# Kernel optimization log

Hardware: AMD Instinct MI355X
Metric: run time of the kernel (lower is better)

## Reference

```python
import jax, jax.numpy as jnp
import numpy as np

B, N, IN, E, OUT = 4, 128, 256, 128, 128
EPS = 1e-5
NEG = -1.0e9


def _ln(x, s, o):
    m = x.mean(-1, keepdims=True)
    v = ((x - m) ** 2).mean(-1, keepdims=True)
    return s * jax.lax.rsqrt(v + EPS) * (x - m) + o


def setup_inputs() -> dict:
    key = jax.random.key(0)
    ks = jax.random.split(key, 30)

    def w(k, i, o):
        return (jax.random.normal(k, (i, o), jnp.float32) / np.sqrt(i)).astype(jnp.float32)

    z_dense = jax.random.normal(ks[0], (B, N, IN), jnp.float32)
    e_dense = jax.random.normal(ks[1], (B, N, N, E), jnp.float32)
    graph_fts = jax.random.normal(ks[2], (B, IN // 2), jnp.float32)
    lengths = jax.random.randint(ks[3], (B,), N // 2, N + 1)
    mask = jnp.arange(N)[None, :] < lengths[:, None]  # (B,N) bool
    adj = jax.random.uniform(ks[4], (B, N, N)) < 0.3
    adj = (adj | jnp.eye(N, dtype=bool)[None]) & mask[:, :, None] & mask[:, None, :]
    return dict(
        z_dense=z_dense, e_dense=e_dense, graph_fts=graph_fts, mask=mask, adj_mat=adj,
        Wt1=w(ks[5], IN, 8), Wt2=w(ks[6], IN, 8), Wt3=w(ks[7], IN, 8),
        We1=w(ks[8], E, 8), We2=w(ks[9], E, 8), We3=w(ks[10], E, 8),
        Wg=w(ks[11], IN // 2, 8),
        Wm1=w(ks[12], IN, OUT), Wm2=w(ks[13], IN, OUT), Wme=w(ks[14], E, OUT), Wmg=w(ks[15], E, OUT),
        ln1_s=jnp.ones((OUT,), jnp.float32), ln1_o=jnp.zeros((OUT,), jnp.float32),
        Wmlp1=w(ks[16], OUT, OUT),
        ln2_s=jnp.ones((OUT,), jnp.float32), ln2_o=jnp.zeros((OUT,), jnp.float32),
        Wmlp2=w(ks[17], OUT, OUT),
        WU1=w(ks[18], IN, OUT), WU2=w(ks[19], OUT, OUT), WU3=w(ks[20], 8, OUT),
        lnf_s=jnp.ones((OUT,), jnp.float32), lnf_o=jnp.zeros((OUT,), jnp.float32),
    )


def reference(z_dense, e_dense, graph_fts, mask, adj_mat,
              Wt1, Wt2, Wt3, We1, We2, We3, Wg,
              Wm1, Wm2, Wme, Wmg,
              ln1_s, ln1_o, Wmlp1, ln2_s, ln2_o, Wmlp2,
              WU1, WU2, WU3, lnf_s, lnf_o):
    mN = mask[..., None]  # (B,N,1)
    # --- triplet messages ---
    tri_1 = jnp.where(mN, z_dense @ Wt1, 0.0)  # (B,N,8)
    tri_2 = jnp.where(mN, z_dense @ Wt2, 0.0)
    tri_3 = jnp.where(mN, z_dense @ Wt3, 0.0)
    tri_e1 = e_dense @ We1  # (B,N,N,8)
    tri_e2 = e_dense @ We2
    tri_e3 = e_dense @ We3
    tri_g = graph_fts @ Wg  # (B,8)
    # (B,N,N,N,8) 7-way broadcast sum (axes: b, i, j, k)
    tri = (tri_1[:, :, None, None, :] + tri_2[:, None, :, None, :] + tri_3[:, None, None, :, :]
           + tri_e1[:, :, :, None, :] + tri_e2[:, :, None, :, :] + tri_e3[:, None, :, :, :]
           + tri_g[:, None, None, None, :])
    msk_tri = mask[:, None, None, :] | mask[:, None, :, None] | mask[:, :, None, None]
    tri = jnp.where(msk_tri[..., None], tri, NEG)
    tri_pooled = tri.max(axis=1)  # (B,N,N,8) -- max over first node axis
    tri_msgs = jax.nn.relu(tri_pooled @ WU3)  # (B,N,N,OUT)

    # --- pairwise messages ---
    msg_1 = jnp.where(mN, z_dense @ Wm1, 0.0)  # (B,N,OUT)
    msg_2 = jnp.where(mN, z_dense @ Wm2, 0.0)
    msg_e = jnp.where(adj_mat[..., None], e_dense @ Wme, 0.0)  # (B,N,N,OUT)
    msg_g = graph_fts @ Wmg  # (B,OUT)
    msgs = msg_1[:, None, :, :] + msg_2[:, :, None, :] + msg_e + msg_g[:, None, None, :]
    # M[-1]: [LN, ReLU, Linear] x2
    x = jax.nn.relu(_ln(msgs, ln1_s, ln1_o)) @ Wmlp1
    x = jax.nn.relu(_ln(x, ln2_s, ln2_o)) @ Wmlp2
    msgs = jnp.where(adj_mat[..., None], x, NEG).max(axis=1)  # (B,N,OUT)

    ret = _ln(z_dense @ WU1 + msgs @ WU2, lnf_s, lnf_o)  # (B,N,OUT)
    return ret, msgs, tri_msgs
```

## Files before the change

### kernel.cpp

```cpp
#include <hip/hip_runtime.h>

#define BN   4
#define NN   128
#define INF  256
#define EF   128
#define OUTF 128
#define EPSF 1e-5f
#define NEGF -998244352.0f

typedef __attribute__((ext_vector_type(8))) short short8;
typedef __attribute__((ext_vector_type(4))) float f32x4;

#define MFMA16(a, b, c) __builtin_amdgcn_mfma_f32_16x16x32_bf16(a, b, c, 0, 0, 0)

__device__ __forceinline__ unsigned short f2bf(float f) {
    unsigned u = __float_as_uint(f);
    u += 0x7fffu + ((u >> 16) & 1u);
    return (unsigned short)(u >> 16);
}
__device__ __forceinline__ unsigned pack2(float a, float b) {
    return (unsigned)f2bf(a) | ((unsigned)f2bf(b) << 16);
}

constexpr size_t TRI1 = 0;
constexpr size_t TRI2 = 4096;
constexpr size_t TRI3 = 8192;
constexpr size_t MSG1 = 12288;
constexpr size_t MSG2 = 77824;
constexpr size_t ZWU1 = 143360;
constexpr size_t TRIG = 208896;
constexpr size_t MSGG = 209920;
constexpr size_t E1T  = 210944;
constexpr size_t E2T  = 735232;
constexpr size_t E3N  = 1259520;
constexpr size_t PREPF = 1783808;

constexpr int W1T_OFF  = 0;
constexpr int W2T_OFF  = 16384;
constexpr int WMET_OFF = 32768;

constexpr size_t O_RET = 0;
constexpr size_t O_MSG = 65536;
constexpr size_t O_TRI = 131072;

__device__ __forceinline__ int detect_int(const void* mask) {
    const unsigned char* m = (const unsigned char*)mask;
    return (m[1] | m[2] | m[3]) == 0 ? 1 : 0;
}
__device__ __forceinline__ bool rdbool(const void* p, size_t idx, int isInt) {
    if (isInt) return ((const int*)p)[idx] != 0;
    return ((const unsigned char*)p)[idx] != 0;
}

__global__ __launch_bounds__(256, 4) void k_pre(
    const float* __restrict__ z, const float* __restrict__ e, const void* __restrict__ mask,
    const float* __restrict__ Wt1, const float* __restrict__ Wt2, const float* __restrict__ Wt3,
    const float* __restrict__ Wm1, const float* __restrict__ Wm2, const float* __restrict__ WU1,
    const float* __restrict__ g, const float* __restrict__ Wg, const float* __restrict__ Wmg,
    const float* __restrict__ W1, const float* __restrict__ W2, const float* __restrict__ Wme,
    const float* __restrict__ We1, const float* __restrict__ We2, const float* __restrict__ We3,
    float* __restrict__ ws, unsigned short* __restrict__ prep)
{
    int bx = blockIdx.x, tid = threadIdx.x;
    __shared__ __align__(16) unsigned char smem[128 * 136 * 2];

    if (bx < 512) {
        unsigned short* Ab = (unsigned short*)smem;
        int bi = bx;
        int b = bi >> 7, i = bi & 127;
        int lane = tid & 63, w = tid >> 6, q = lane >> 4, n = lane & 15;
        {
            int half = lane >> 5, c4 = (lane & 31) * 4;
            #pragma unroll
            for (int it = 0; it < 16; it++) {
                int row = 32 * w + 2 * it + half;
                float4 v = *(const float4*)(e + (size_t)bi * 16384 + (size_t)row * 128 + c4);
                unsigned* dst = (unsigned*)&Ab[row * 136 + c4];
                dst[0] = pack2(v.x, v.y);
                dst[1] = pack2(v.z, v.w);
            }
        }
        short8 bfrag[4][2];
        {
            #pragma unroll
            for (int t = 0; t < 2; t++) {
                int col = 16 * t + n;
                const float* Wsel = (col < 8) ? We1 : (col < 16 ? We2 : We3);
                int csel = col & 7;
                float mval = (col < 24) ? 1.f : 0.f;
                #pragma unroll
                for (int ks = 0; ks < 4; ks++) {
                    union { short8 s; unsigned short u[8]; } tmp;
                    #pragma unroll
                    for (int jj = 0; jj < 8; jj++) {
                        int k = ks * 32 + q * 8 + jj;
                        tmp.u[jj] = f2bf(Wsel[k * 8 + csel] * mval);
                    }
                    bfrag[ks][t] = tmp.s;
                }
            }
        }
        __builtin_amdgcn_wave_barrier();

        f32x4 ac2[2][2];
        #pragma unroll
        for (int rt = 0; rt < 2; rt++)
            #pragma unroll
            for (int t = 0; t < 2; t++) ac2[rt][t] = 0.f;
        #pragma unroll
        for (int ks = 0; ks < 4; ks++) {
            int k0 = ks * 32 + q * 8;
            short8 a0 = *(const short8*)&Ab[(32 * w + n) * 136 + k0];
            short8 a1 = *(const short8*)&Ab[(32 * w + 16 + n) * 136 + k0];
            #pragma unroll
            for (int t = 0; t < 2; t++) {
                ac2[0][t] = MFMA16(a0, bfrag[ks][t], ac2[0][t]);
                ac2[1][t] = MFMA16(a1, bfrag[ks][t], ac2[1][t]);
            }
        }
        #pragma unroll
        for (int rt = 0; rt < 2; rt++)
            #pragma unroll
            for (int reg = 0; reg < 4; reg++) {
                int row = 32 * w + 16 * rt + 4 * q + reg;
                float v0 = ac2[rt][0][reg];
                if (n < 8) ws[E1T + ((size_t)(b * 128 + row) * 128 + i) * 8 + n] = v0;
                else       ws[E2T + ((size_t)(b * 128 + row) * 128 + i) * 8 + (n - 8)] = v0;
                if (n < 8) ws[E3N + ((size_t)bi * 128 + row) * 8 + n] = ac2[rt][1][reg];
            }
        return;
    }
    if (bx < 1024) {
        int bn = bx - 512;
        int isInt = detect_int(mask);
        float* zr = (float*)smem;
        zr[tid] = z[(size_t)bn * INF + tid];
        __syncthreads();
        float mk = rdbool(mask, bn, isInt) ? 1.f : 0.f;
        for (int idx = tid; idx < 408; idx += 256) {
            const float* W; int c; size_t dst; int width; bool msk;
            if (idx < 8)        { W = Wt1; c = idx;       dst = TRI1 + (size_t)bn * 8;   width = 8;   msk = true;  }
            else if (idx < 16)  { W = Wt2; c = idx - 8;   dst = TRI2 + (size_t)bn * 8;   width = 8;   msk = true;  }
            else if (idx < 24)  { W = Wt3; c = idx - 16;  dst = TRI3 + (size_t)bn * 8;   width = 8;   msk = true;  }
            else if (idx < 152) { W = Wm1; c = idx - 24;  dst = MSG1 + (size_t)bn * 128; width = 128; msk = true;  }
            else if (idx < 280) { W = Wm2; c = idx - 152; dst = MSG2 + (size_t)bn * 128; width = 128; msk = true;  }
            else                { W = WU1; c = idx - 280; dst = ZWU1 + (size_t)bn * 128; width = 128; msk = false; }
            float a0 = 0.f, a1 = 0.f;
            #pragma unroll 8
            for (int k = 0; k < INF; k += 2) {
                a0 += zr[k] * W[k * width + c];
                a1 += zr[k + 1] * W[(k + 1) * width + c];
            }
            float acc = a0 + a1;
            ws[dst + c] = msk ? acc * mk : acc;
        }
        return;
    }
    if (bx < 1028) {
        int b = bx - 1024;
        float* gr = (float*)smem;
        if (tid < 128) gr[tid] = g[b * 128 + tid];
        __syncthreads();
        if (tid < 8) {
            float a = 0.f;
            for (int k = 0; k < 128; k++) a += gr[k] * Wg[k * 8 + tid];
            ws[TRIG + b * 8 + tid] = a;
        } else if (tid >= 128) {
            int c = tid - 128;
            float a = 0.f;
            for (int k = 0; k < 128; k++) a += gr[k] * Wmg[k * 128 + c];
            ws[MSGG + b * 128 + c] = a;
        }
        return;
    }
    {
        int idx = (bx - 1028) * 256 + tid;
        const float* W = (idx < 16384) ? W1 : (idx < 32768 ? W2 : Wme);
        int local = idx & 16383;
        int f = local >> 3, jj = local & 7;
        int lane = f & 63, fg = f >> 6;
        int t = fg & 7, ks = fg >> 3;
        int n = lane & 15, q = lane >> 4;
        int row = 16 * t + n;
        int k = ks * 32 + q * 8 + jj;
        prep[idx] = f2bf(W[k * 128 + row]);
    }
}

constexpr int PQSTR = 268;

__global__ __launch_bounds__(256, 4) void k_main(
    const float* __restrict__ e, const void* __restrict__ mask, const void* __restrict__ adj,
    const float* __restrict__ ln1s, const float* __restrict__ ln1o,
    const float* __restrict__ ln2s, const float* __restrict__ ln2o,
    const unsigned short* __restrict__ prep, const float* __restrict__ WU3,
    float* __restrict__ ws, float* __restrict__ out)
{
    int bx = blockIdx.x, tid = threadIdx.x;
    int gct = bx / 3, r3 = bx - gct * 3;
    __shared__ __align__(16) unsigned char smem[128 * 136 * 2 + 2048];
    int lane = tid & 63, w = tid >> 6, q = lane >> 4, n = lane & 15;

    if (r3 == 2) {
        int g = gct;
        int j0 = ((g >> 3) & 7) * 16, k0 = (g & 7) * 16, b = g >> 6;
        int isInt = detect_int(mask);
        float* Pl = (float*)smem;
        float* Ql = (float*)(smem + 16 * PQSTR * 4);
        float* pooled = (float*)smem;
        __shared__ unsigned char mloc[128];
        if (tid < 128) mloc[tid] = rdbool(mask, b * 128 + tid, isInt) ? 1 : 0;

        int col4 = (tid & 31) * 4, rowgrp = tid >> 5;
        float4 wvr[8];
        #pragma unroll
        for (int c = 0; c < 8; c++) wvr[c] = *(const float4*)(WU3 + c * 128 + col4);

        int tj = tid >> 4, tk = tid & 15;
        f32x4 accM[2], accU[2];
        accM[0] = NEGF; accM[1] = NEGF; accU[0] = NEGF; accU[1] = NEGF;

        for (int i0 = 0; i0 < 128; i0 += 32) {
            __syncthreads();
            {
                float4 t1c = *(const float4*)(ws + TRI1 + (size_t)b * 1024 + i0 * 8 + lane * 4);
                #pragma unroll
                for (int r4 = 0; r4 < 4; r4++) {
                    int row = 4 * w + r4;
                    float4 ev = *(const float4*)(ws + E1T + (size_t)(b * 128 + j0 + row) * 1024 + i0 * 8 + lane * 4);
                    float4 qv = *(const float4*)(ws + E2T + (size_t)(b * 128 + k0 + row) * 1024 + i0 * 8 + lane * 4);
                    float4 pv;
                    pv.x = ev.x + t1c.x; pv.y = ev.y + t1c.y;
                    pv.z = ev.z + t1c.z; pv.w = ev.w + t1c.w;
                    *(float4*)(Pl + row * PQSTR + lane * 4) = pv;
                    *(float4*)(Ql + row * PQSTR + lane * 4) = qv;
                }
            }
            __syncthreads();
            const float* pp = Pl + tj * PQSTR;
            const float* qq = Ql + tk * PQSTR;
            for (int ii = 0; ii < 32; ii++) {
                bool m_i = mloc[i0 + ii] != 0;
                f32x4 p0 = *(const f32x4*)(pp + ii * 8);
                f32x4 p1 = *(const f32x4*)(pp + ii * 8 + 4);
                f32x4 q0 = *(const f32x4*)(qq + ii * 8);
                f32x4 q1 = *(const f32x4*)(qq + ii * 8 + 4);
                f32x4 v0 = p0 + q0;
                f32x4 v1 = p1 + q1;
                if (m_i) {
                    accM[0] = __builtin_elementwise_max(accM[0], v0);
                    accM[1] = __builtin_elementwise_max(accM[1], v1);
                } else {
                    accU[0] = __builtin_elementwise_max(accU[0], v0);
                    accU[1] = __builtin_elementwise_max(accU[1], v1);
                }
            }
        }
        f32x4 sel[2];
        {
            bool all_i = (mloc[j0 + tj] | mloc[k0 + tk]) != 0;
            if (all_i) {
                sel[0] = __builtin_elementwise_max(accM[0], accU[0]);
                sel[1] = __builtin_elementwise_max(accM[1], accU[1]);
            } else {
                sel[0] = accM[0]; sel[1] = accM[1];
            }
        }
        __syncthreads();
        {
            const float* t2 = ws + TRI2 + (size_t)(b * 128 + j0 + tj) * 8;
            const float* t3 = ws + TRI3 + (size_t)(b * 128 + k0 + tk) * 8;
            const float* e3 = ws + E3N + ((size_t)(b * 128 + j0 + tj) * 128 + (k0 + tk)) * 8;
            const float* tg = ws + TRIG + (size_t)b * 8;
            #pragma unroll
            for (int c = 0; c < 8; c++)
                pooled[c * 260 + tid] = sel[c >> 2][c & 3] + t2[c] + t3[c] + e3[c] + tg[c];
        }
        __syncthreads();
        #pragma unroll
        for (int pass = 0; pass < 32; pass++) {
            int p = pass * 8 + rowgrp;
            float4 s = { 0.f, 0.f, 0.f, 0.f };
            #pragma unroll
            for (int c = 0; c < 8; c++) {
                float pv = pooled[c * 260 + p];
                s.x += pv * wvr[c].x; s.y += pv * wvr[c].y;
                s.z += pv * wvr[c].z; s.w += pv * wvr[c].w;
            }
            s.x = fmaxf(s.x, 0.f); s.y = fmaxf(s.y, 0.f);
            s.z = fmaxf(s.z, 0.f); s.w = fmaxf(s.w, 0.f);
            int pj = p >> 4, pk = p & 15;
            *(float4*)(out + O_TRI + ((size_t)(b * 128 + j0 + pj) * 128 + (k0 + pk)) * 128 + col4) = s;
        }
        return;
    }

    unsigned short* Ab = (unsigned short*)smem;
    float* pw = (float*)(smem + 128 * 136 * 2);
    int bj = gct * 2 + r3;
    int b = bj >> 7, j = bj & 127;
    int isInt = detect_int(mask);

    {
        int half = lane >> 5, c4 = (lane & 31) * 4;
        #pragma unroll
        for (int it = 0; it < 16; it++) {
            int row = 32 * w + 2 * it + half;
            float4 v = *(const float4*)(e + (((size_t)b * 128 + row) * 128 + j) * 128 + c4);
            unsigned* dst = (unsigned*)&Ab[row * 136 + c4];
            dst[0] = pack2(v.x, v.y);
            dst[1] = pack2(v.z, v.w);
        }
    }
    __builtin_amdgcn_wave_barrier();

    f32x4 acc[2][8];
    #pragma unroll
    for (int rt = 0; rt < 2; rt++)
        #pragma unroll
        for (int t = 0; t < 8; t++) acc[rt][t] = 0.f;

    #pragma unroll
    for (int ks = 0; ks < 4; ks++) {
        int k0 = ks * 32 + q * 8;
        short8 a0 = *(const short8*)&Ab[(32 * w + n) * 136 + k0];
        short8 a1 = *(const short8*)&Ab[(32 * w + 16 + n) * 136 + k0];
        #pragma unroll
        for (int t = 0; t < 8; t++) {
            short8 bt = *(const short8*)&prep[WMET_OFF + ((ks * 8 + t) * 64 + lane) * 8];
            acc[0][t] = MFMA16(a0, bt, acc[0][t]);
            acc[1][t] = MFMA16(a1, bt, acc[1][t]);
        }
    }

    float msum[8];
    #pragma unroll
    for (int t = 0; t < 8; t++)
        msum[t] = ws[MSG1 + (size_t)bj * 128 + 16 * t + n] + ws[MSGG + (size_t)b * 128 + 16 * t + n];
    float adjm[2][4];
    float rs[2][4], rss[2][4];
    #pragma unroll
    for (int rt = 0; rt < 2; rt++)
        #pragma unroll
        for (int reg = 0; reg < 4; reg++) {
            int row = 32 * w + 16 * rt + 4 * q + reg;
            bool av = rdbool(adj, ((size_t)b * 128 + row) * 128 + j, isInt);
            adjm[rt][reg] = av ? 1.f : 0.f;
            float s = 0.f, ssq = 0.f;
            #pragma unroll
            for (int t = 0; t < 8; t++) {
                float v = acc[rt][t][reg] * adjm[rt][reg]
                        + ws[MSG2 + ((size_t)b * 128 + row) * 128 + 16 * t + n] + msum[t];
                acc[rt][t][reg] = v;
                s += v; ssq += v * v;
            }
            rs[rt][reg] = s; rss[rt][reg] = ssq;
        }
    #pragma unroll
    for (int d = 1; d < 16; d <<= 1) {
        #pragma unroll
        for (int rt = 0; rt < 2; rt++)
            #pragma unroll
            for (int reg = 0; reg < 4; reg++) {
                rs[rt][reg]  += __shfl_xor(rs[rt][reg], d, 64);
                rss[rt][reg] += __shfl_xor(rss[rt][reg], d, 64);
            }
    }
    {
        float s1v[8], o1v[8];
        #pragma unroll
        for (int t = 0; t < 8; t++) { s1v[t] = ln1s[16 * t + n]; o1v[t] = ln1o[16 * t + n]; }
        #pragma unroll
        for (int rt = 0; rt < 2; rt++)
            #pragma unroll
            for (int reg = 0; reg < 4; reg++) {
                float mu = rs[rt][reg] * (1.f / 128);
                float inv = rsqrtf(rss[rt][reg] * (1.f / 128) - mu * mu + EPSF);
                int row = 32 * w + 16 * rt + 4 * q + reg;
                #pragma unroll
                for (int t = 0; t < 8; t++) {
                    float v = fmaxf(s1v[t] * inv * (acc[rt][t][reg] - mu) + o1v[t], 0.f);
                    Ab[row * 136 + 16 * t + n] = f2bf(v);
                }
            }
    }
    __builtin_amdgcn_wave_barrier();

    #pragma unroll
    for (int rt = 0; rt < 2; rt++)
        #pragma unroll
        for (int t = 0; t < 8; t++) acc[rt][t] = 0.f;
    #pragma unroll
    for (int ks = 0; ks < 4; ks++) {
        int k0 = ks * 32 + q * 8;
        short8 a0 = *(const short8*)&Ab[(32 * w + n) * 136 + k0];
        short8 a1 = *(const short8*)&Ab[(32 * w + 16 + n) * 136 + k0];
        #pragma unroll
        for (int t = 0; t < 8; t++) {
            short8 bt = *(const short8*)&prep[W1T_OFF + ((ks * 8 + t) * 64 + lane) * 8];
            acc[0][t] = MFMA16(a0, bt, acc[0][t]);
            acc[1][t] = MFMA16(a1, bt, acc[1][t]);
        }
    }
    #pragma unroll
    for (int rt = 0; rt < 2; rt++)
        #pragma unroll
        for (int reg = 0; reg < 4; reg++) {
            float s = 0.f, ssq = 0.f;
            #pragma unroll
            for (int t = 0; t < 8; t++) { float v = acc[rt][t][reg]; s += v; ssq += v * v; }
            rs[rt][reg] = s; rss[rt][reg] = ssq;
        }
    #pragma unroll
    for (int d = 1; d < 16; d <<= 1) {
        #pragma unroll
        for (int rt = 0; rt < 2; rt++)
            #pragma unroll
            for (int reg = 0; reg < 4; reg++) {
                rs[rt][reg]  += __shfl_xor(rs[rt][reg], d, 64);
                rss[rt][reg] += __shfl_xor(rss[rt][reg], d, 64);
            }
    }
    {
        float s2v[8], o2v[8];
        #pragma unroll
        for (int t = 0; t < 8; t++) { s2v[t] = ln2s[16 * t + n]; o2v[t] = ln2o[16 * t + n]; }
        #pragma unroll
        for (int rt = 0; rt < 2; rt++)
            #pragma unroll
            for (int reg = 0; reg < 4; reg++) {
                float mu = rs[rt][reg] * (1.f / 128);
                float inv = rsqrtf(rss[rt][reg] * (1.f / 128) - mu * mu + EPSF);
                int row = 32 * w + 16 * rt + 4 * q + reg;
                #pragma unroll
                for (int t = 0; t < 8; t++) {
                    float v = fmaxf(s2v[t] * inv * (acc[rt][t][reg] - mu) + o2v[t], 0.f);
                    Ab[row * 136 + 16 * t + n] = f2bf(v);
                }
            }
    }
    __builtin_amdgcn_wave_barrier();

    #pragma unroll
    for (int rt = 0; rt < 2; rt++)
        #pragma unroll
        for (int t = 0; t < 8; t++) acc[rt][t] = 0.f;
    #pragma unroll
    for (int ks = 0; ks < 4; ks++) {
        int k0 = ks * 32 + q * 8;
        short8 a0 = *(const short8*)&Ab[(32 * w + n) * 136 + k0];
        short8 a1 = *(const short8*)&Ab[(32 * w + 16 + n) * 136 + k0];
        #pragma unroll
        for (int t = 0; t < 8; t++) {
            short8 bt = *(const short8*)&prep[W2T_OFF + ((ks * 8 + t) * 64 + lane) * 8];
            acc[0][t] = MFMA16(a0, bt, acc[0][t]);
            acc[1][t] = MFMA16(a1, bt, acc[1][t]);
        }
    }
    float colmax[8];
    #pragma unroll
    for (int t = 0; t < 8; t++) colmax[t] = NEGF;
    #pragma unroll
    for (int rt = 0; rt < 2; rt++)
        #pragma unroll
        for (int reg = 0; reg < 4; reg++) {
            if (adjm[rt][reg] > 0.f) {
                #pragma unroll
                for (int t = 0; t < 8; t++) colmax[t] = fmaxf(colmax[t], acc[rt][t][reg]);
            }
        }
    #pragma unroll
    for (int t = 0; t < 8; t++) {
        colmax[t] = fmaxf(colmax[t], __shfl_xor(colmax[t], 16, 64));
        colmax[t] = fmaxf(colmax[t], __shfl_xor(colmax[t], 32, 64));
    }
    if (lane < 16) {
        #pragma unroll
        for (int t = 0; t < 8; t++) pw[w * 128 + 16 * t + lane] = colmax[t];
    }
    __syncthreads();
    if (tid < 128) {
        float mx = fmaxf(fmaxf(pw[tid], pw[128 + tid]), fmaxf(pw[256 + tid], pw[384 + tid]));
        out[O_MSG + (size_t)bj * 128 + tid] = mx;
    }
}

__global__ __launch_bounds__(128) void k_final(
    const float* __restrict__ ws, const float* __restrict__ WU2,
    const float* __restrict__ lnfs, const float* __restrict__ lnfo,
    float* __restrict__ out)
{
    int bn = blockIdx.x, tid = threadIdx.x;
    __shared__ float mrow[128];
    __shared__ float red[4];
    mrow[tid] = out[O_MSG + (size_t)bn * 128 + tid];
    __syncthreads();
    float y = ws[ZWU1 + (size_t)bn * 128 + tid];
    #pragma unroll 8
    for (int k = 0; k < 128; k++) y += mrow[k] * WU2[k * 128 + tid];
    float s = y, ss = y * y;
    for (int d = 1; d < 64; d <<= 1) { s += __shfl_xor(s, d, 64); ss += __shfl_xor(ss, d, 64); }
    if ((tid & 63) == 0) { red[(tid >> 6) * 2] = s; red[(tid >> 6) * 2 + 1] = ss; }
    __syncthreads();
    float S = red[0] + red[2], SS = red[1] + red[3];
    float m_ = S * (1.f / 128), v_ = SS * (1.f / 128) - m_ * m_;
    float r = rsqrtf(v_ + EPSF);
    out[O_RET + (size_t)bn * 128 + tid] = lnfs[tid] * r * (y - m_) + lnfo[tid];
}

extern "C" void kernel_launch(void* const* d_in, const int* in_sizes, int n_in,
                              void* d_out, int out_size, void* d_ws, size_t ws_size,
                              hipStream_t stream)
{
    const float* z    = (const float*)d_in[0];
    const float* e    = (const float*)d_in[1];
    const float* gf   = (const float*)d_in[2];
    const void*  mask = d_in[3];
    const void*  adj  = d_in[4];
    const float* Wt1 = (const float*)d_in[5];
    const float* Wt2 = (const float*)d_in[6];
    const float* Wt3 = (const float*)d_in[7];
    const float* We1 = (const float*)d_in[8];
    const float* We2 = (const float*)d_in[9];
    const float* We3 = (const float*)d_in[10];
    const float* Wg  = (const float*)d_in[11];
    const float* Wm1 = (const float*)d_in[12];
    const float* Wm2 = (const float*)d_in[13];
    const float* Wme = (const float*)d_in[14];
    const float* Wmg = (const float*)d_in[15];
    const float* ln1s = (const float*)d_in[16];
    const float* ln1o = (const float*)d_in[17];
    const float* W1   = (const float*)d_in[18];
    const float* ln2s = (const float*)d_in[19];
    const float* ln2o = (const float*)d_in[20];
    const float* W2   = (const float*)d_in[21];
    const float* WU1  = (const float*)d_in[22];
    const float* WU2  = (const float*)d_in[23];
    const float* WU3  = (const float*)d_in[24];
    const float* lnfs = (const float*)d_in[25];
    const float* lnfo = (const float*)d_in[26];
    float* out = (float*)d_out;
    float* ws  = (float*)d_ws;
    unsigned short* prep = (unsigned short*)(ws + PREPF);

    hipLaunchKernelGGL(k_pre, dim3(1220), dim3(256), 0, stream,
                       z, e, mask, Wt1, Wt2, Wt3, Wm1, Wm2, WU1, gf, Wg, Wmg,
                       W1, W2, Wme, We1, We2, We3, ws, prep);
    hipLaunchKernelGGL(k_main, dim3(768), dim3(256), 0, stream,
                       e, mask, adj, ln1s, ln1o, ln2s, ln2o, prep, WU3, ws, out);
    hipLaunchKernelGGL(k_final, dim3(512), dim3(128), 0, stream,
                       ws, WU2, lnfs, lnfo, out);
}
```

Measured before the change: 192.9 us.

## Split message MLP blocks in half, repartition triplet max across waves

The pairwise message blocks now each handle 64 of the 128 source rows instead of all 128. That halves shared memory and accumulator registers per block and raises the grid from 768 to 1280 blocks; the two half-maxima go to workspace and are combined in k_final. The triplet blocks come first in the grid and split the i range across wave pairs with per-wave LDS staging and wave barriers instead of block syncs. tri_1 is folded into E1T inside k_pre, and k_final's matvec uses two accumulators. This adds a workspace round trip for partial maxima and more complex triplet indexing.

```diff
diff --git a/kernel.cpp b/kernel.cpp
--- a/kernel.cpp
+++ b/kernel.cpp
@@ -33,7 +33,8 @@
 constexpr size_t E1T  = 210944;
 constexpr size_t E2T  = 735232;
 constexpr size_t E3N  = 1259520;
-constexpr size_t PREPF = 1783808;
+constexpr size_t PM0  = 1783808;
+constexpr size_t PREPF = 1914880;
 
 constexpr int W1T_OFF  = 0;
 constexpr int W2T_OFF  = 16384;
@@ -79,6 +80,19 @@
                 dst[0] = pack2(v.x, v.y);
                 dst[1] = pack2(v.z, v.w);
             }
+        }
+        float t1v;
+        {
+            int c = lane & 7, kk = lane >> 3;
+            const float* zr = z + (size_t)bi * INF;
+            float s = 0.f;
+            #pragma unroll
+            for (int m = 0; m < 32; m++) s = fmaf(zr[kk * 32 + m], Wt1[(kk * 32 + m) * 8 + c], s);
+            s += __shfl_xor(s, 8, 64);
+            s += __shfl_xor(s, 16, 64);
+            s += __shfl_xor(s, 32, 64);
+            int isInt = detect_int(mask);
+            t1v = rdbool(mask, bi, isInt) ? s : 0.f;
         }
         short8 bfrag[4][2];
         {
@@ -124,7 +138,7 @@
             for (int reg = 0; reg < 4; reg++) {
                 int row = 32 * w + 16 * rt + 4 * q + reg;
                 float v0 = ac2[rt][0][reg];
-                if (n < 8) ws[E1T + ((size_t)(b * 128 + row) * 128 + i) * 8 + n] = v0;
+                if (n < 8) ws[E1T + ((size_t)(b * 128 + row) * 128 + i) * 8 + n] = v0 + t1v;
                 else       ws[E2T + ((size_t)(b * 128 + row) * 128 + i) * 8 + (n - 8)] = v0;
                 if (n < 8) ws[E3N + ((size_t)bi * 128 + row) * 8 + n] = ac2[rt][1][reg];
             }
@@ -187,8 +201,6 @@
     }
 }
 
-constexpr int PQSTR = 268;
-
 __global__ __launch_bounds__(256, 4) void k_main(
     const float* __restrict__ e, const void* __restrict__ mask, const void* __restrict__ adj,
     const float* __restrict__ ln1s, const float* __restrict__ ln1o,
@@ -197,84 +209,108 @@
     float* __restrict__ ws, float* __restrict__ out)
 {
     int bx = blockIdx.x, tid = threadIdx.x;
-    int gct = bx / 3, r3 = bx - gct * 3;
-    __shared__ __align__(16) unsigned char smem[128 * 136 * 2 + 2048];
+    __shared__ __align__(16) unsigned char smem[64 * 136 * 2 + 2048];
     int lane = tid & 63, w = tid >> 6, q = lane >> 4, n = lane & 15;
-
-    if (r3 == 2) {
-        int g = gct;
+    int isInt = detect_int(mask);
+
+    if (bx < 256) {
+        int g = bx;
         int j0 = ((g >> 3) & 7) * 16, k0 = (g & 7) * 16, b = g >> 6;
-        int isInt = detect_int(mask);
-        float* Pl = (float*)smem;
-        float* Ql = (float*)(smem + 16 * PQSTR * 4);
+        int wi = w >> 1, wc = w & 1;
+        int tj = lane >> 3, tk = lane & 7;
+        int col4 = (tid & 31) * 4, rowgrp = tid >> 5;
+
+        unsigned long long mball = __ballot(rdbool(mask, (size_t)b * 128 + wi * 64 + lane, isInt));
+
+        float* Pb = (float*)smem + w * 1152;
+        float* Qb = Pb + 576;
+
+        f32x4 aM[2][2], aU[2][2];
+        #pragma unroll
+        for (int jj = 0; jj < 2; jj++)
+            #pragma unroll
+            for (int kk = 0; kk < 2; kk++) { aM[jj][kk] = NEGF; aU[jj][kk] = NEGF; }
+
+        for (int ch = 0; ch < 8; ch++) {
+            int ibase = wi * 64 + ch * 8;
+            #pragma unroll
+            for (int r = 0; r < 2; r++) {
+                int f = r * 64 + lane;
+                int jr = f >> 3, ii = f & 7;
+                f32x4 pv = *(const f32x4*)(ws + E1T + (size_t)(b * 128 + j0 + jr) * 1024 + (ibase + ii) * 8 + wc * 4);
+                f32x4 qv = *(const f32x4*)(ws + E2T + (size_t)(b * 128 + k0 + jr) * 1024 + (ibase + ii) * 8 + wc * 4);
+                *(f32x4*)(Pb + jr * 36 + ii * 4) = pv;
+                *(f32x4*)(Qb + jr * 36 + ii * 4) = qv;
+            }
+            __builtin_amdgcn_wave_barrier();
+            #pragma unroll
+            for (int ii = 0; ii < 8; ii++) {
+                f32x4 p0 = *(const f32x4*)(Pb + tj * 36 + ii * 4);
+                f32x4 p1 = *(const f32x4*)(Pb + (tj + 8) * 36 + ii * 4);
+                f32x4 q0 = *(const f32x4*)(Qb + tk * 36 + ii * 4);
+                f32x4 q1 = *(const f32x4*)(Qb + (tk + 8) * 36 + ii * 4);
+                f32x4 v00 = p0 + q0, v01 = p0 + q1, v10 = p1 + q0, v11 = p1 + q1;
+                if ((mball >> (ch * 8 + ii)) & 1) {
+                    aM[0][0] = __builtin_elementwise_max(aM[0][0], v00);
+                    aM[0][1] = __builtin_elementwise_max(aM[0][1], v01);
+                    aM[1][0] = __builtin_elementwise_max(aM[1][0], v10);
+                    aM[1][1] = __builtin_elementwise_max(aM[1][1], v11);
+                } else {
+                    aU[0][0] = __builtin_elementwise_max(aU[0][0], v00);
+                    aU[0][1] = __builtin_elementwise_max(aU[0][1], v01);
+                    aU[1][0] = __builtin_elementwise_max(aU[1][0], v10);
+                    aU[1][1] = __builtin_elementwise_max(aU[1][1], v11);
+                }
+            }
+        }
+        {
+            bool mj[2], mk2[2];
+            mj[0]  = rdbool(mask, (size_t)b * 128 + j0 + tj, isInt);
+            mj[1]  = rdbool(mask, (size_t)b * 128 + j0 + tj + 8, isInt);
+            mk2[0] = rdbool(mask, (size_t)b * 128 + k0 + tk, isInt);
+            mk2[1] = rdbool(mask, (size_t)b * 128 + k0 + tk + 8, isInt);
+            #pragma unroll
+            for (int jj = 0; jj < 2; jj++)
+                #pragma unroll
+                for (int kk = 0; kk < 2; kk++)
+                    if (mj[jj] | mk2[kk])
+                        aM[jj][kk] = __builtin_elementwise_max(aM[jj][kk], aU[jj][kk]);
+        }
+        __syncthreads();
         float* pooled = (float*)smem;
-        __shared__ unsigned char mloc[128];
-        if (tid < 128) mloc[tid] = rdbool(mask, b * 128 + tid, isInt) ? 1 : 0;
-
-        int col4 = (tid & 31) * 4, rowgrp = tid >> 5;
         float4 wvr[8];
         #pragma unroll
         for (int c = 0; c < 8; c++) wvr[c] = *(const float4*)(WU3 + c * 128 + col4);
 
-        int tj = tid >> 4, tk = tid & 15;
-        f32x4 accM[2], accU[2];
-        accM[0] = NEGF; accM[1] = NEGF; accU[0] = NEGF; accU[1] = NEGF;
-
-        for (int i0 = 0; i0 < 128; i0 += 32) {
-            __syncthreads();
-            {
-                float4 t1c = *(const float4*)(ws + TRI1 + (size_t)b * 1024 + i0 * 8 + lane * 4);
+        if (wi == 0) {
+            #pragma unroll
+            for (int jj = 0; jj < 2; jj++)
                 #pragma unroll
-                for (int r4 = 0; r4 < 4; r4++) {
-                    int row = 4 * w + r4;
-                    float4 ev = *(const float4*)(ws + E1T + (size_t)(b * 128 + j0 + row) * 1024 + i0 * 8 + lane * 4);
-                    float4 qv = *(const float4*)(ws + E2T + (size_t)(b * 128 + k0 + row) * 1024 + i0 * 8 + lane * 4);
-                    float4 pv;
-                    pv.x = ev.x + t1c.x; pv.y = ev.y + t1c.y;
-                    pv.z = ev.z + t1c.z; pv.w = ev.w + t1c.w;
-                    *(float4*)(Pl + row * PQSTR + lane * 4) = pv;
-                    *(float4*)(Ql + row * PQSTR + lane * 4) = qv;
+                for (int kk = 0; kk < 2; kk++) {
+                    int p = (tj + 8 * jj) * 16 + (tk + 8 * kk);
+                    #pragma unroll
+                    for (int cc = 0; cc < 4; cc++)
+                        pooled[(wc * 4 + cc) * 260 + p] = aM[jj][kk][cc];
                 }
-            }
-            __syncthreads();
-            const float* pp = Pl + tj * PQSTR;
-            const float* qq = Ql + tk * PQSTR;
-            for (int ii = 0; ii < 32; ii++) {
-                bool m_i = mloc[i0 + ii] != 0;
-                f32x4 p0 = *(const f32x4*)(pp + ii * 8);
-                f32x4 p1 = *(const f32x4*)(pp + ii * 8 + 4);
-                f32x4 q0 = *(const f32x4*)(qq + ii * 8);
-                f32x4 q1 = *(const f32x4*)(qq + ii * 8 + 4);
-                f32x4 v0 = p0 + q0;
-                f32x4 v1 = p1 + q1;
-                if (m_i) {
-                    accM[0] = __builtin_elementwise_max(accM[0], v0);
-                    accM[1] = __builtin_elementwise_max(accM[1], v1);
-                } else {
-                    accU[0] = __builtin_elementwise_max(accU[0], v0);
-                    accU[1] = __builtin_elementwise_max(accU[1], v1);
+        }
+        __syncthreads();
+        if (wi == 1) {
+            const float* tg = ws + TRIG + (size_t)b * 8 + wc * 4;
+            #pragma unroll
+            for (int jj = 0; jj < 2; jj++)
+                #pragma unroll
+                for (int kk = 0; kk < 2; kk++) {
+                    int jv = j0 + tj + 8 * jj, kv = k0 + tk + 8 * kk;
+                    const float* t2 = ws + TRI2 + (size_t)(b * 128 + jv) * 8 + wc * 4;
+                    const float* t3 = ws + TRI3 + (size_t)(b * 128 + kv) * 8 + wc * 4;
+                    const float* e3 = ws + E3N + ((size_t)(b * 128 + jv) * 128 + kv) * 8 + wc * 4;
+                    int p = (tj + 8 * jj) * 16 + (tk + 8 * kk);
+                    #pragma unroll
+                    for (int cc = 0; cc < 4; cc++) {
+                        int idx = (wc * 4 + cc) * 260 + p;
+                        pooled[idx] = fmaxf(pooled[idx], aM[jj][kk][cc]) + t2[cc] + t3[cc] + e3[cc] + tg[cc];
+                    }
                 }
-            }
-        }
-        f32x4 sel[2];
-        {
-            bool all_i = (mloc[j0 + tj] | mloc[k0 + tk]) != 0;
-            if (all_i) {
-                sel[0] = __builtin_elementwise_max(accM[0], accU[0]);
-                sel[1] = __builtin_elementwise_max(accM[1], accU[1]);
-            } else {
-                sel[0] = accM[0]; sel[1] = accM[1];
-            }
-        }
-        __syncthreads();
-        {
-            const float* t2 = ws + TRI2 + (size_t)(b * 128 + j0 + tj) * 8;
-            const float* t3 = ws + TRI3 + (size_t)(b * 128 + k0 + tk) * 8;
-            const float* e3 = ws + E3N + ((size_t)(b * 128 + j0 + tj) * 128 + (k0 + tk)) * 8;
-            const float* tg = ws + TRIG + (size_t)b * 8;
-            #pragma unroll
-            for (int c = 0; c < 8; c++)
-                pooled[c * 260 + tid] = sel[c >> 2][c & 3] + t2[c] + t3[c] + e3[c] + tg[c];
         }
         __syncthreads();
         #pragma unroll
@@ -296,17 +332,17 @@
     }
 
     unsigned short* Ab = (unsigned short*)smem;
-    float* pw = (float*)(smem + 128 * 136 * 2);
-    int bj = gct * 2 + r3;
+    float* pw = (float*)(smem + 64 * 136 * 2);
+    int pb = bx - 256;
+    int bj = pb >> 1, hb = pb & 1;
     int b = bj >> 7, j = bj & 127;
-    int isInt = detect_int(mask);
 
     {
         int half = lane >> 5, c4 = (lane & 31) * 4;
         #pragma unroll
-        for (int it = 0; it < 16; it++) {
-            int row = 32 * w + 2 * it + half;
-            float4 v = *(const float4*)(e + (((size_t)b * 128 + row) * 128 + j) * 128 + c4);
+        for (int it = 0; it < 8; it++) {
+            int row = 16 * w + 2 * it + half;
+            float4 v = *(const float4*)(e + (((size_t)b * 128 + hb * 64 + row) * 128 + j) * 128 + c4);
             unsigned* dst = (unsigned*)&Ab[row * 136 + c4];
             dst[0] = pack2(v.x, v.y);
             dst[1] = pack2(v.z, v.w);
@@ -314,22 +350,17 @@
     }
     __builtin_amdgcn_wave_barrier();
 
-    f32x4 acc[2][8];
-    #pragma unroll
-    for (int rt = 0; rt < 2; rt++)
-        #pragma unroll
-        for (int t = 0; t < 8; t++) acc[rt][t] = 0.f;
-
+    f32x4 acc[8];
+    #pragma unroll
+    for (int t = 0; t < 8; t++) acc[t] = 0.f;
     #pragma unroll
     for (int ks = 0; ks < 4; ks++) {
-        int k0 = ks * 32 + q * 8;
-        short8 a0 = *(const short8*)&Ab[(32 * w + n) * 136 + k0];
-        short8 a1 = *(const short8*)&Ab[(32 * w + 16 + n) * 136 + k0];
+        int kf = ks * 32 + q * 8;
+        short8 a0 = *(const short8*)&Ab[(16 * w + n) * 136 + kf];
         #pragma unroll
         for (int t = 0; t < 8; t++) {
             short8 bt = *(const short8*)&prep[WMET_OFF + ((ks * 8 + t) * 64 + lane) * 8];
-            acc[0][t] = MFMA16(a0, bt, acc[0][t]);
-            acc[1][t] = MFMA16(a1, bt, acc[1][t]);
+            acc[t] = MFMA16(a0, bt, acc[t]);
         }
     }
 
@@ -337,138 +368,116 @@
     #pragma unroll
     for (int t = 0; t < 8; t++)
         msum[t] = ws[MSG1 + (size_t)bj * 128 + 16 * t + n] + ws[MSGG + (size_t)b * 128 + 16 * t + n];
-    float adjm[2][4];
-    float rs[2][4], rss[2][4];
-    #pragma unroll
-    for (int rt = 0; rt < 2; rt++)
+    float adjm[4];
+    float rs[4], rss[4];
+    #pragma unroll
+    for (int reg = 0; reg < 4; reg++) {
+        int gi = hb * 64 + 16 * w + 4 * q + reg;
+        bool av = rdbool(adj, ((size_t)b * 128 + gi) * 128 + j, isInt);
+        adjm[reg] = av ? 1.f : 0.f;
+        float s = 0.f, ssq = 0.f;
+        #pragma unroll
+        for (int t = 0; t < 8; t++) {
+            float v = acc[t][reg] * adjm[reg]
+                    + ws[MSG2 + ((size_t)b * 128 + gi) * 128 + 16 * t + n] + msum[t];
+            acc[t][reg] = v;
+            s += v; ssq += v * v;
+        }
+        rs[reg] = s; rss[reg] = ssq;
+    }
+    #pragma unroll
+    for (int d = 1; d < 16; d <<= 1) {
         #pragma unroll
         for (int reg = 0; reg < 4; reg++) {
-            int row = 32 * w + 16 * rt + 4 * q + reg;
-            bool av = rdbool(adj, ((size_t)b * 128 + row) * 128 + j, isInt);
-            adjm[rt][reg] = av ? 1.f : 0.f;
-            float s = 0.f, ssq = 0.f;
-            #pragma unroll
-            for (int t = 0; t < 8; t++) {
-                float v = acc[rt][t][reg] * adjm[rt][reg]
-                        + ws[MSG2 + ((size_t)b * 128 + row) * 128 + 16 * t + n] + msum[t];
-                acc[rt][t][reg] = v;
-                s += v; ssq += v * v;
-            }
-            rs[rt][reg] = s; rss[rt][reg] = ssq;
-        }
-    #pragma unroll
-    for (int d = 1; d < 16; d <<= 1) {
-        #pragma unroll
-        for (int rt = 0; rt < 2; rt++)
-            #pragma unroll
-            for (int reg = 0; reg < 4; reg++) {
-                rs[rt][reg]  += __shfl_xor(rs[rt][reg], d, 64);
-                rss[rt][reg] += __shfl_xor(rss[rt][reg], d, 64);
-            }
+            rs[reg]  += __shfl_xor(rs[reg], d, 64);
+            rss[reg] += __shfl_xor(rss[reg], d, 64);
+        }
     }
     {
         float s1v[8], o1v[8];
         #pragma unroll
         for (int t = 0; t < 8; t++) { s1v[t] = ln1s[16 * t + n]; o1v[t] = ln1o[16 * t + n]; }
         #pragma unroll
-        for (int rt = 0; rt < 2; rt++)
-            #pragma unroll
-            for (int reg = 0; reg < 4; reg++) {
-                float mu = rs[rt][reg] * (1.f / 128);
-                float inv = rsqrtf(rss[rt][reg] * (1.f / 128) - mu * mu + EPSF);
-                int row = 32 * w + 16 * rt + 4 * q + reg;
-                #pragma unroll
-                for (int t = 0; t < 8; t++) {
-                    float v = fmaxf(s1v[t] * inv * (acc[rt][t][reg] - mu) + o1v[t], 0.f);
-                    Ab[row * 136 + 16 * t + n] = f2bf(v);
-                }
-            }
+        for (int reg = 0; reg < 4; reg++) {
+            float mu = rs[reg] * (1.f / 128);
+            float inv = rsqrtf(rss[reg] * (1.f / 128) - mu * mu + EPSF);
+            int row = 16 * w + 4 * q + reg;
+            #pragma unroll
+            for (int t = 0; t < 8; t++) {
+                float v = fmaxf(s1v[t] * inv * (acc[t][reg] - mu) + o1v[t], 0.f);
+                Ab[row * 136 + 16 * t + n] = f2bf(v);
+            }
+        }
     }
     __builtin_amdgcn_wave_barrier();
 
     #pragma unroll
-    for (int rt = 0; rt < 2; rt++)
-        #pragma unroll
-        for (int t = 0; t < 8; t++) acc[rt][t] = 0.f;
+    for (int t = 0; t < 8; t++) acc[t] = 0.f;
     #pragma unroll
     for (int ks = 0; ks < 4; ks++) {
-        int k0 = ks * 32 + q * 8;
-        short8 a0 = *(const short8*)&Ab[(32 * w + n) * 136 + k0];
-        short8 a1 = *(const short8*)&Ab[(32 * w + 16 + n) * 136 + k0];
+        int kf = ks * 32 + q * 8;
+        short8 a0 = *(const short8*)&Ab[(16 * w + n) * 136 + kf];
         #pragma unroll
         for (int t = 0; t < 8; t++) {
             short8 bt = *(const short8*)&prep[W1T_OFF + ((ks * 8 + t) * 64 + lane) * 8];
-            acc[0][t] = MFMA16(a0, bt, acc[0][t]);
-            acc[1][t] = MFMA16(a1, bt, acc[1][t]);
-        }
-    }
-    #pragma unroll
-    for (int rt = 0; rt < 2; rt++)
+            acc[t] = MFMA16(a0, bt, acc[t]);
+        }
+    }
+    #pragma unroll
+    for (int reg = 0; reg < 4; reg++) {
+        float s = 0.f, ssq = 0.f;
+        #pragma unroll
+        for (int t = 0; t < 8; t++) { float v = acc[t][reg]; s += v; ssq += v * v; }
+        rs[reg] = s; rss[reg] = ssq;
+    }
+    #pragma unroll
+    for (int d = 1; d < 16; d <<= 1) {
         #pragma unroll
         for (int reg = 0; reg < 4; reg++) {
-            float s = 0.f, ssq = 0.f;
-            #pragma unroll
-            for (int t = 0; t < 8; t++) { float v = acc[rt][t][reg]; s += v; ssq += v * v; }
-            rs[rt][reg] = s; rss[rt][reg] = ssq;
-        }
-    #pragma unroll
-    for (int d = 1; d < 16; d <<= 1) {
-        #pragma unroll
-        for (int rt = 0; rt < 2; rt++)
-            #pragma unroll
-            for (int reg = 0; reg < 4; reg++) {
-                rs[rt][reg]  += __shfl_xor(rs[rt][reg], d, 64);
-                rss[rt][reg] += __shfl_xor(rss[rt][reg], d, 64);
-            }
+            rs[reg]  += __shfl_xor(rs[reg], d, 64);
+            rss[reg] += __shfl_xor(rss[reg], d, 64);
+        }
     }
     {
         float s2v[8], o2v[8];
         #pragma unroll
         for (int t = 0; t < 8; t++) { s2v[t] = ln2s[16 * t + n]; o2v[t] = ln2o[16 * t + n]; }
         #pragma unroll
-        for (int rt = 0; rt < 2; rt++)
-            #pragma unroll
-            for (int reg = 0; reg < 4; reg++) {
-                float mu = rs[rt][reg] * (1.f / 128);
-                float inv = rsqrtf(rss[rt][reg] * (1.f / 128) - mu * mu + EPSF);
-                int row = 32 * w + 16 * rt + 4 * q + reg;
-                #pragma unroll
-                for (int t = 0; t < 8; t++) {
-                    float v = fmaxf(s2v[t] * inv * (acc[rt][t][reg] - mu) + o2v[t], 0.f);
-                    Ab[row * 136 + 16 * t + n] = f2bf(v);
-                }
-            }
+        for (int reg = 0; reg < 4; reg++) {
+            float mu = rs[reg] * (1.f / 128);
+            float inv = rsqrtf(rss[reg] * (1.f / 128) - mu * mu + EPSF);
+            int row = 16 * w + 4 * q + reg;
+            #pragma unroll
+            for (int t = 0; t < 8; t++) {
+                float v = fmaxf(s2v[t] * inv * (acc[t][reg] - mu) + o2v[t], 0.f);
+                Ab[row * 136 + 16 * t + n] = f2bf(v);
+            }
+        }
     }
     __builtin_amdgcn_wave_barrier();
 
     #pragma unroll
-    for (int rt = 0; rt < 2; rt++)
-        #pragma unroll
-        for (int t = 0; t < 8; t++) acc[rt][t] = 0.f;
+    for (int t = 0; t < 8; t++) acc[t] = 0.f;
     #pragma unroll
     for (int ks = 0; ks < 4; ks++) {
-        int k0 = ks * 32 + q * 8;
-        short8 a0 = *(const short8*)&Ab[(32 * w + n) * 136 + k0];
-        short8 a1 = *(const short8*)&Ab[(32 * w + 16 + n) * 136 + k0];
+        int kf = ks * 32 + q * 8;
+        short8 a0 = *(const short8*)&Ab[(16 * w + n) * 136 + kf];
         #pragma unroll
         for (int t = 0; t < 8; t++) {
             short8 bt = *(const short8*)&prep[W2T_OFF + ((ks * 8 + t) * 64 + lane) * 8];
-            acc[0][t] = MFMA16(a0, bt, acc[0][t]);
-            acc[1][t] = MFMA16(a1, bt, acc[1][t]);
+            acc[t] = MFMA16(a0, bt, acc[t]);
         }
     }
     float colmax[8];
     #pragma unroll
     for (int t = 0; t < 8; t++) colmax[t] = NEGF;
     #pragma unroll
-    for (int rt = 0; rt < 2; rt++)
-        #pragma unroll
-        for (int reg = 0; reg < 4; reg++) {
-            if (adjm[rt][reg] > 0.f) {
-                #pragma unroll
-                for (int t = 0; t < 8; t++) colmax[t] = fmaxf(colmax[t], acc[rt][t][reg]);
-            }
-        }
+    for (int reg = 0; reg < 4; reg++) {
+        if (adjm[reg] > 0.f) {
+            #pragma unroll
+            for (int t = 0; t < 8; t++) colmax[t] = fmaxf(colmax[t], acc[t][reg]);
+        }
+    }
     #pragma unroll
     for (int t = 0; t < 8; t++) {
         colmax[t] = fmaxf(colmax[t], __shfl_xor(colmax[t], 16, 64));
@@ -481,7 +490,7 @@
     __syncthreads();
     if (tid < 128) {
         float mx = fmaxf(fmaxf(pw[tid], pw[128 + tid]), fmaxf(pw[256 + tid], pw[384 + tid]));
-        out[O_MSG + (size_t)bj * 128 + tid] = mx;
+        ws[PM0 + (size_t)hb * 65536 + (size_t)bj * 128 + tid] = mx;
     }
 }
 
@@ -493,11 +502,18 @@
     int bn = blockIdx.x, tid = threadIdx.x;
     __shared__ float mrow[128];
     __shared__ float red[4];
-    mrow[tid] = out[O_MSG + (size_t)bn * 128 + tid];
+    float mx = fmaxf(ws[PM0 + (size_t)bn * 128 + tid], ws[PM0 + 65536 + (size_t)bn * 128 + tid]);
+    mrow[tid] = mx;
+    out[O_MSG + (size_t)bn * 128 + tid] = mx;
     __syncthreads();
     float y = ws[ZWU1 + (size_t)bn * 128 + tid];
+    float a0 = 0.f, a1 = 0.f;
     #pragma unroll 8
-    for (int k = 0; k < 128; k++) y += mrow[k] * WU2[k * 128 + tid];
+    for (int k = 0; k < 128; k += 2) {
+        a0 = fmaf(mrow[k], WU2[k * 128 + tid], a0);
+        a1 = fmaf(mrow[k + 1], WU2[(k + 1) * 128 + tid], a1);
+    }
+    y += a0 + a1;
     float s = y, ss = y * y;
     for (int d = 1; d < 64; d <<= 1) { s += __shfl_xor(s, d, 64); ss += __shfl_xor(ss, d, 64); }
     if ((tid & 63) == 0) { red[(tid >> 6) * 2] = s; red[(tid >> 6) * 2 + 1] = ss; }
@@ -546,7 +562,7 @@
     hipLaunchKernelGGL(k_pre, dim3(1220), dim3(256), 0, stream,
                        z, e, mask, Wt1, Wt2, Wt3, Wm1, Wm2, WU1, gf, Wg, Wmg,
                        W1, W2, Wme, We1, We2, We3, ws, prep);
-    hipLaunchKernelGGL(k_main, dim3(768), dim3(256), 0, stream,
+    hipLaunchKernelGGL(k_main, dim3(1280), dim3(256), 0, stream,
                        e, mask, adj, ln1s, ln1o, ln2s, ln2o, prep, WU3, ws, out);
     hipLaunchKernelGGL(k_final, dim3(512), dim3(128), 0, stream,
                        ws, WU2, lnfs, lnfo, out);
```

After: 192.8 us. No clear change (-0.1%).
